# Optimization experiments

Hardware: AMD Instinct MI355X
Metric: run time of the kernel (lower is better)

Reference implementation:

```python
import jax, jax.numpy as jnp
import numpy as np

B, C = 4096, 10000
TAU = 1.0
MIN_K, MAX_K = 30, 100


def setup_inputs() -> dict:
    key = jax.random.key(0)
    k1, k2 = jax.random.split(key, 2)
    logit = jax.random.normal(k1, (B, C), dtype=jnp.float32)
    target = jax.random.randint(k2, (B,), 0, C)
    # long-tailed class counts: exponential decay from 1000 down to 5
    cls_num = np.exp(np.linspace(np.log(1000.0), np.log(5.0), C)).astype(np.float32)
    cls_num_ratio = cls_num / cls_num.sum()
    log_cls_num = jnp.asarray(np.log(cls_num_ratio + 1e-6), dtype=jnp.float32)
    freq = (cls_num.max() / cls_num).astype(np.float32)
    freq_norm = (freq - freq.min()) / (freq.max() - freq.min() + 1e-6)
    k_per_class = jnp.asarray((freq_norm * (MAX_K - MIN_K) + MIN_K).astype(np.int32))
    return {"logit": logit, "target": target, "log_cls_num": log_cls_num,
            "k_per_class": k_per_class}


def reference(logit, target, log_cls_num, k_per_class):
    b, c = logit.shape
    rows = jnp.arange(b)
    # logit-adjusted cross entropy (loss_full)
    logit_adj = logit + TAU * log_cls_num[None, :]
    log_p_adj = jax.nn.log_softmax(logit_adj, axis=1)  # [B, C]
    loss_full = -jnp.mean(log_p_adj[rows, target])
    # per-row variable-k top-k mask on the ORIGINAL logits
    prob_adj = jnp.exp(log_p_adj)
    k = jnp.minimum(k_per_class[target], c)            # [B]
    sorted_desc = -jnp.sort(-logit, axis=1)            # [B, C] descending
    thresh = sorted_desc[rows, k - 1]                  # k-th largest per row
    mask = logit >= thresh[:, None]
    masked_prob = jnp.where(mask, prob_adj, 0.0) + 1e-6
    masked_prob = masked_prob / masked_prob.sum(axis=1, keepdims=True)
    loss_topk = -jnp.mean(jnp.log(masked_prob)[rows, target])
    return 0.5 * loss_full + 0.5 * loss_topk
```

## Files before the change

kernel.cpp:

```cpp
#include <hip/hip_runtime.h>

#define BLOCK 256
#define WPB 4
#define C_DIM 10000
#define C4 (C_DIM / 4)
#define NIT4 ((C4 + 63) / 64)
#define TAU 1.0f
#define CAP 512
#define PIV_HI 2.0f
#define PIV_LO 1.0f

__device__ __forceinline__ unsigned flip_key(float f) {
    unsigned u = __float_as_uint(f);
    return (u & 0x80000000u) ? ~u : (u | 0x80000000u);
}
__device__ __forceinline__ float unflip_key(unsigned k) {
    unsigned u = (k & 0x80000000u) ? (k & 0x7fffffffu) : ~k;
    return __uint_as_float(u);
}
__device__ __forceinline__ int mbcnt64(unsigned long long m) {
    return (int)__builtin_amdgcn_mbcnt_hi((unsigned)(m >> 32),
               __builtin_amdgcn_mbcnt_lo((unsigned)(m & 0xffffffffu), 0u));
}

__global__ void zero_out_kernel(float* out, int n) {
    int i = blockIdx.x * blockDim.x + threadIdx.x;
    if (i < n) out[i] = 0.f;
}

__device__ __forceinline__ void wave_pick(uint4 hv, int lane, int shift,
                                          unsigned& prefix, unsigned& kr, unsigned& cnt) {
    unsigned loc = hv.x + hv.y + hv.z + hv.w;
    unsigned suf = loc;
    #pragma unroll
    for (int off = 1; off < 64; off <<= 1) {
        unsigned o = (unsigned)__shfl_down((int)suf, off);
        if (lane + off < 64) suf += o;
    }
    unsigned sufex = suf - loc;
    unsigned s3 = sufex + hv.w;
    unsigned s2 = s3 + hv.z;
    unsigned s1 = s2 + hv.y;
    unsigned s0 = s1 + hv.x;
    int bsel = -1; unsigned nkr = 0u, ncnt = 0u;
    if      (s3 >= kr && s3 - hv.w < kr) { bsel = 4 * lane + 3; nkr = kr - (s3 - hv.w); ncnt = hv.w; }
    else if (s2 >= kr && s2 - hv.z < kr) { bsel = 4 * lane + 2; nkr = kr - (s2 - hv.z); ncnt = hv.z; }
    else if (s1 >= kr && s1 - hv.y < kr) { bsel = 4 * lane + 1; nkr = kr - (s1 - hv.y); ncnt = hv.y; }
    else if (s0 >= kr && s0 - hv.x < kr) { bsel = 4 * lane + 0; nkr = kr - (s0 - hv.x); ncnt = hv.x; }
    unsigned long long pm = __ballot(bsel >= 0);
    int src = __ffsll((unsigned long long)pm) - 1;
    prefix |= ((unsigned)__shfl(bsel, src)) << shift;
    kr  = (unsigned)__shfl((int)nkr, src);
    cnt = (unsigned)__shfl((int)ncnt, src);
}

__global__ __launch_bounds__(BLOCK, 4) void topk_la_loss_kernel(
    const float* __restrict__ logit, const int* __restrict__ target,
    const float* __restrict__ lcn, const int* __restrict__ kpc,
    float* __restrict__ out, int B) {
    __shared__ unsigned candk[WPB][CAP];
    __shared__ unsigned short candi[WPB][CAP];
    __shared__ unsigned hist[WPB][256];

    const int tid = threadIdx.x;
    const int lane = tid & 63;
    const int wid = tid >> 6;
    const int row = blockIdx.x * WPB + wid;
    if (row >= B) return;

    const float* lrow = logit + (size_t)row * C_DIM;
    unsigned* ck = candk[wid];
    unsigned short* ci = candi[wid];
    unsigned* h = hist[wid];

    const int t = target[row];
    int k = kpc[t]; if (k > C_DIM) k = C_DIM;

    float z = 0.f, madj = -__builtin_inff();
    unsigned nb = 0u;
    #pragma unroll 2
    for (int it = 0; it < NIT4; ++it) {
        const int j4 = it * 64 + lane;
        float4 f, l;
        if (j4 < C4) {
            f = ((const float4*)lrow)[j4];
            l = ((const float4*)lcn)[j4];
        } else {
            f = make_float4(-1e30f, -1e30f, -1e30f, -1e30f);
            l = make_float4(0.f, 0.f, 0.f, 0.f);
        }
        const float a0 = f.x + TAU * l.x, a1 = f.y + TAU * l.y;
        const float a2 = f.z + TAU * l.z, a3 = f.w + TAU * l.w;
        z += __expf(a0) + __expf(a1) + __expf(a2) + __expf(a3);
        madj = fmaxf(madj, fmaxf(fmaxf(a0, a1), fmaxf(a2, a3)));
        const int j = 4 * j4;
        unsigned long long m;
        m = __ballot(f.x >= PIV_HI);
        if (f.x >= PIV_HI) { unsigned p = nb + (unsigned)mbcnt64(m); if (p < CAP) { ck[p] = __float_as_uint(f.x); ci[p] = (unsigned short)(j + 0); } }
        nb += (unsigned)__popcll(m);
        m = __ballot(f.y >= PIV_HI);
        if (f.y >= PIV_HI) { unsigned p = nb + (unsigned)mbcnt64(m); if (p < CAP) { ck[p] = __float_as_uint(f.y); ci[p] = (unsigned short)(j + 1); } }
        nb += (unsigned)__popcll(m);
        m = __ballot(f.z >= PIV_HI);
        if (f.z >= PIV_HI) { unsigned p = nb + (unsigned)mbcnt64(m); if (p < CAP) { ck[p] = __float_as_uint(f.z); ci[p] = (unsigned short)(j + 2); } }
        nb += (unsigned)__popcll(m);
        m = __ballot(f.w >= PIV_HI);
        if (f.w >= PIV_HI) { unsigned p = nb + (unsigned)mbcnt64(m); if (p < CAP) { ck[p] = __float_as_uint(f.w); ci[p] = (unsigned short)(j + 3); } }
        nb += (unsigned)__popcll(m);
    }
    #pragma unroll
    for (int off = 32; off; off >>= 1) madj = fmaxf(madj, __shfl_xor(madj, off));

    unsigned n = nb;
    int path = (n >= (unsigned)k && n <= CAP) ? 0 : ((n < (unsigned)k) ? 1 : 2);

    if (path == 1) {
        nb = 0u;
        for (int it = 0; it < NIT4; ++it) {
            const int j4 = it * 64 + lane;
            float4 f;
            if (j4 < C4) f = ((const float4*)lrow)[j4];
            else f = make_float4(-1e30f, -1e30f, -1e30f, -1e30f);
            const int j = 4 * j4;
            unsigned long long m;
            m = __ballot(f.x >= PIV_LO);
            if (f.x >= PIV_LO) { unsigned p = nb + (unsigned)mbcnt64(m); if (p < CAP) { ck[p] = __float_as_uint(f.x); ci[p] = (unsigned short)(j + 0); } }
            nb += (unsigned)__popcll(m);
            m = __ballot(f.y >= PIV_LO);
            if (f.y >= PIV_LO) { unsigned p = nb + (unsigned)mbcnt64(m); if (p < CAP) { ck[p] = __float_as_uint(f.y); ci[p] = (unsigned short)(j + 1); } }
            nb += (unsigned)__popcll(m);
            m = __ballot(f.z >= PIV_LO);
            if (f.z >= PIV_LO) { unsigned p = nb + (unsigned)mbcnt64(m); if (p < CAP) { ck[p] = __float_as_uint(f.z); ci[p] = (unsigned short)(j + 2); } }
            nb += (unsigned)__popcll(m);
            m = __ballot(f.w >= PIV_LO);
            if (f.w >= PIV_LO) { unsigned p = nb + (unsigned)mbcnt64(m); if (p < CAP) { ck[p] = __float_as_uint(f.w); ci[p] = (unsigned short)(j + 3); } }
            nb += (unsigned)__popcll(m);
        }
        n = nb;
        path = (n >= (unsigned)k && n <= CAP) ? 0 : 2;
    }

    float thresh;
    if (path == 0) {
        const int nc = (int)n;
        unsigned prefix = 0u, kr = (unsigned)k, cnt = n, kmask = 0u;
        for (int q = 0; q < 4; ++q) {
            if (cnt == 1u) break;
            const int shift = 24 - 8 * q;
            *(uint4*)&h[4 * lane] = make_uint4(0u, 0u, 0u, 0u);
            for (int i = lane; i < nc; i += 64) {
                unsigned kk = ck[i];
                if ((kk & kmask) == prefix) atomicAdd(&h[(kk >> shift) & 0xFFu], 1u);
            }
            uint4 hv = *(const uint4*)&h[4 * lane];
            wave_pick(hv, lane, shift, prefix, kr, cnt);
            kmask |= (0xFFu << shift);
        }
        if (cnt == 1u && kmask != 0xFFFFFFFFu) {
            unsigned found = 0u;
            for (int i = lane; i < nc; i += 64) {
                unsigned kk = ck[i];
                if ((kk & kmask) == prefix) found = kk;
            }
            #pragma unroll
            for (int off = 32; off; off >>= 1) found |= (unsigned)__shfl_xor((int)found, off);
            prefix = found;
        }
        thresh = __uint_as_float(prefix);
    } else {
        unsigned prefix = 0u, kr = (unsigned)k, cnt = 0u;
        for (int p = 0; p < 4; ++p) {
            const int shift = 24 - 8 * p;
            const unsigned pmask = p ? (0xFFFFFFFFu << (shift + 8)) : 0u;
            *(uint4*)&h[4 * lane] = make_uint4(0u, 0u, 0u, 0u);
            for (int it = 0; it < NIT4; ++it) {
                const int j4 = it * 64 + lane;
                if (j4 < C4) {
                    float4 f = ((const float4*)lrow)[j4];
                    unsigned kk;
                    kk = flip_key(f.x); if ((kk & pmask) == prefix) atomicAdd(&h[(kk >> shift) & 0xFFu], 1u);
                    kk = flip_key(f.y); if ((kk & pmask) == prefix) atomicAdd(&h[(kk >> shift) & 0xFFu], 1u);
                    kk = flip_key(f.z); if ((kk & pmask) == prefix) atomicAdd(&h[(kk >> shift) & 0xFFu], 1u);
                    kk = flip_key(f.w); if ((kk & pmask) == prefix) atomicAdd(&h[(kk >> shift) & 0xFFu], 1u);
                }
            }
            uint4 hv = *(const uint4*)&h[4 * lane];
            wave_pick(hv, lane, shift, prefix, kr, cnt);
        }
        thresh = unflip_key(prefix);
    }

    const bool rare = fabsf(madj) > 80.f;
    float sm = 0.f;
    if (!rare) {
        if (path == 0) {
            const int nc = (int)n;
            for (int i = lane; i < nc; i += 64) {
                const float v = __uint_as_float(ck[i]);
                if (v >= thresh) sm += __expf(v + TAU * lcn[ci[i]]);
            }
        } else {
            for (int it = 0; it < NIT4; ++it) {
                const int j4 = it * 64 + lane;
                if (j4 < C4) {
                    float4 f = ((const float4*)lrow)[j4];
                    float4 l = ((const float4*)lcn)[j4];
                    if (f.x >= thresh) sm += __expf(f.x + TAU * l.x);
                    if (f.y >= thresh) sm += __expf(f.y + TAU * l.y);
                    if (f.z >= thresh) sm += __expf(f.z + TAU * l.z);
                    if (f.w >= thresh) sm += __expf(f.w + TAU * l.w);
                }
            }
        }
    } else {
        z = 0.f;
        for (int it = 0; it < NIT4; ++it) {
            const int j4 = it * 64 + lane;
            if (j4 < C4) {
                float4 f = ((const float4*)lrow)[j4];
                float4 l = ((const float4*)lcn)[j4];
                float e;
                e = __expf(f.x + TAU * l.x - madj); z += e; if (f.x >= thresh) sm += e;
                e = __expf(f.y + TAU * l.y - madj); z += e; if (f.y >= thresh) sm += e;
                e = __expf(f.z + TAU * l.z - madj); z += e; if (f.z >= thresh) sm += e;
                e = __expf(f.w + TAU * l.w - madj); z += e; if (f.w >= thresh) sm += e;
            }
        }
    }

    #pragma unroll
    for (int off = 32; off; off >>= 1) {
        z  += __shfl_down(z, off);
        sm += __shfl_down(sm, off);
    }
    if (lane == 0) {
        const float Z = z, S = sm;
        const float logit_t = lrow[t];
        const float adj_t = logit_t + TAU * lcn[t];
        const float sub = rare ? madj : 0.f;
        const float lpt = adj_t - sub - __logf(Z);
        const float p_num = ((logit_t >= thresh) ? __expf(lpt) : 0.f) + 1e-6f;
        const float Smask = S / Z + (float)C_DIM * 1e-6f;
        const float loss = 0.5f * (-lpt + __logf(Smask) - __logf(p_num));
        atomicAdd(out, loss / (float)B);
    }
}

extern "C" void kernel_launch(void* const* d_in, const int* in_sizes, int n_in,
                              void* d_out, int out_size, void* d_ws, size_t ws_size,
                              hipStream_t stream) {
    const float* logit  = (const float*)d_in[0];
    const int*   target = (const int*)d_in[1];
    const float* lcn    = (const float*)d_in[2];
    const int*   kpc    = (const int*)d_in[3];
    float* out = (float*)d_out;
    const int B = in_sizes[1];

    zero_out_kernel<<<1, 64, 0, stream>>>(out, out_size);
    const int nblk = (B + WPB - 1) / WPB;
    topk_la_loss_kernel<<<nblk, BLOCK, 0, stream>>>(logit, target, lcn, kpc, out, B);
}
```

Before: 286.7 us.

## Split each row across four waves with block-level candidate merge

Each row now gets a full block of four waves instead of one wave. Each wave scans a quarter of the columns and collects its own threshold candidates, and shared-memory reductions then combine the max, candidate counts, Z and S. Wave 0 alone selects the threshold over the merged candidate lists. Launch bounds also change to allow more blocks per CU. This adds block syncs, and wave 0 runs the radix selection while the other three waves sit idle. The fallback full-row histogram path also runs on one wave only.

```diff
diff --git a/kernel.cpp b/kernel.cpp
--- a/kernel.cpp
+++ b/kernel.cpp
@@ -4,6 +4,8 @@
 #define WPB 4
 #define C_DIM 10000
 #define C4 (C_DIM / 4)
+#define SEGQ (C4 / WPB)
+#define ITQ ((SEGQ + 63) / 64)
 #define NIT4 ((C4 + 63) / 64)
 #define TAU 1.0f
 #define CAP 512
@@ -54,37 +56,39 @@
     cnt = (unsigned)__shfl((int)ncnt, src);
 }
 
-__global__ __launch_bounds__(BLOCK, 4) void topk_la_loss_kernel(
+__global__ __launch_bounds__(BLOCK, 8) void topk_la_loss_kernel(
     const float* __restrict__ logit, const int* __restrict__ target,
     const float* __restrict__ lcn, const int* __restrict__ kpc,
     float* __restrict__ out, int B) {
     __shared__ unsigned candk[WPB][CAP];
     __shared__ unsigned short candi[WPB][CAP];
-    __shared__ unsigned hist[WPB][256];
+    __shared__ unsigned hist[256];
+    __shared__ unsigned sh_nb[WPB];
+    __shared__ float red_a[WPB], red_b[WPB];
+    __shared__ float sh_thresh;
 
     const int tid = threadIdx.x;
     const int lane = tid & 63;
     const int wid = tid >> 6;
-    const int row = blockIdx.x * WPB + wid;
-    if (row >= B) return;
-
+    const int row = blockIdx.x;
     const float* lrow = logit + (size_t)row * C_DIM;
+
+    const int t = target[row];
+    int k = kpc[t]; if (k > C_DIM) k = C_DIM;
+
     unsigned* ck = candk[wid];
     unsigned short* ci = candi[wid];
-    unsigned* h = hist[wid];
-
-    const int t = target[row];
-    int k = kpc[t]; if (k > C_DIM) k = C_DIM;
+    const int base4 = wid * SEGQ;
 
     float z = 0.f, madj = -__builtin_inff();
     unsigned nb = 0u;
     #pragma unroll 2
-    for (int it = 0; it < NIT4; ++it) {
-        const int j4 = it * 64 + lane;
+    for (int it = 0; it < ITQ; ++it) {
+        const int j4l = it * 64 + lane;
         float4 f, l;
-        if (j4 < C4) {
-            f = ((const float4*)lrow)[j4];
-            l = ((const float4*)lcn)[j4];
+        if (j4l < SEGQ) {
+            f = ((const float4*)lrow)[base4 + j4l];
+            l = ((const float4*)lcn)[base4 + j4l];
         } else {
             f = make_float4(-1e30f, -1e30f, -1e30f, -1e30f);
             l = make_float4(0.f, 0.f, 0.f, 0.f);
@@ -93,7 +97,7 @@
         const float a2 = f.z + TAU * l.z, a3 = f.w + TAU * l.w;
         z += __expf(a0) + __expf(a1) + __expf(a2) + __expf(a3);
         madj = fmaxf(madj, fmaxf(fmaxf(a0, a1), fmaxf(a2, a3)));
-        const int j = 4 * j4;
+        const int j = 4 * (base4 + j4l);
         unsigned long long m;
         m = __ballot(f.x >= PIV_HI);
         if (f.x >= PIV_HI) { unsigned p = nb + (unsigned)mbcnt64(m); if (p < CAP) { ck[p] = __float_as_uint(f.x); ci[p] = (unsigned short)(j + 0); } }
@@ -110,18 +114,23 @@
     }
     #pragma unroll
     for (int off = 32; off; off >>= 1) madj = fmaxf(madj, __shfl_xor(madj, off));
-
-    unsigned n = nb;
-    int path = (n >= (unsigned)k && n <= CAP) ? 0 : ((n < (unsigned)k) ? 1 : 2);
+    if (lane == 0) { red_a[wid] = madj; sh_nb[wid] = nb; }
+    __syncthreads();
+
+    const float madjB = fmaxf(fmaxf(red_a[0], red_a[1]), fmaxf(red_a[2], red_a[3]));
+    unsigned nbs0 = sh_nb[0], nbs1 = sh_nb[1], nbs2 = sh_nb[2], nbs3 = sh_nb[3];
+    unsigned ntot = nbs0 + nbs1 + nbs2 + nbs3;
+    unsigned nmax = max(max(nbs0, nbs1), max(nbs2, nbs3));
+    int path = (ntot >= (unsigned)k && nmax <= CAP) ? 0 : ((ntot < (unsigned)k) ? 1 : 2);
 
     if (path == 1) {
         nb = 0u;
-        for (int it = 0; it < NIT4; ++it) {
-            const int j4 = it * 64 + lane;
+        for (int it = 0; it < ITQ; ++it) {
+            const int j4l = it * 64 + lane;
             float4 f;
-            if (j4 < C4) f = ((const float4*)lrow)[j4];
+            if (j4l < SEGQ) f = ((const float4*)lrow)[base4 + j4l];
             else f = make_float4(-1e30f, -1e30f, -1e30f, -1e30f);
-            const int j = 4 * j4;
+            const int j = 4 * (base4 + j4l);
             unsigned long long m;
             m = __ballot(f.x >= PIV_LO);
             if (f.x >= PIV_LO) { unsigned p = nb + (unsigned)mbcnt64(m); if (p < CAP) { ck[p] = __float_as_uint(f.x); ci[p] = (unsigned short)(j + 0); } }
@@ -136,75 +145,90 @@
             if (f.w >= PIV_LO) { unsigned p = nb + (unsigned)mbcnt64(m); if (p < CAP) { ck[p] = __float_as_uint(f.w); ci[p] = (unsigned short)(j + 3); } }
             nb += (unsigned)__popcll(m);
         }
-        n = nb;
-        path = (n >= (unsigned)k && n <= CAP) ? 0 : 2;
-    }
-
-    float thresh;
+        if (lane == 0) sh_nb[wid] = nb;
+        __syncthreads();
+        nbs0 = sh_nb[0]; nbs1 = sh_nb[1]; nbs2 = sh_nb[2]; nbs3 = sh_nb[3];
+        ntot = nbs0 + nbs1 + nbs2 + nbs3;
+        nmax = max(max(nbs0, nbs1), max(nbs2, nbs3));
+        path = (ntot >= (unsigned)k && nmax <= CAP) ? 0 : 2;
+    }
+
     if (path == 0) {
-        const int nc = (int)n;
-        unsigned prefix = 0u, kr = (unsigned)k, cnt = n, kmask = 0u;
-        for (int q = 0; q < 4; ++q) {
-            if (cnt == 1u) break;
-            const int shift = 24 - 8 * q;
-            *(uint4*)&h[4 * lane] = make_uint4(0u, 0u, 0u, 0u);
-            for (int i = lane; i < nc; i += 64) {
-                unsigned kk = ck[i];
-                if ((kk & kmask) == prefix) atomicAdd(&h[(kk >> shift) & 0xFFu], 1u);
-            }
-            uint4 hv = *(const uint4*)&h[4 * lane];
-            wave_pick(hv, lane, shift, prefix, kr, cnt);
-            kmask |= (0xFFu << shift);
-        }
-        if (cnt == 1u && kmask != 0xFFFFFFFFu) {
-            unsigned found = 0u;
-            for (int i = lane; i < nc; i += 64) {
-                unsigned kk = ck[i];
-                if ((kk & kmask) == prefix) found = kk;
-            }
-            #pragma unroll
-            for (int off = 32; off; off >>= 1) found |= (unsigned)__shfl_xor((int)found, off);
-            prefix = found;
-        }
-        thresh = __uint_as_float(prefix);
+        if (wid == 0) {
+            unsigned prefix = 0u, kr = (unsigned)k, cnt = ntot, kmask = 0u;
+            const unsigned nbs[4] = {nbs0, nbs1, nbs2, nbs3};
+            for (int q = 0; q < 4; ++q) {
+                if (cnt == 1u) break;
+                const int shift = 24 - 8 * q;
+                *(uint4*)&hist[4 * lane] = make_uint4(0u, 0u, 0u, 0u);
+                #pragma unroll
+                for (int s = 0; s < 4; ++s) {
+                    for (int i = lane; i < (int)nbs[s]; i += 64) {
+                        unsigned kk = candk[s][i];
+                        if ((kk & kmask) == prefix) atomicAdd(&hist[(kk >> shift) & 0xFFu], 1u);
+                    }
+                }
+                uint4 hv = *(const uint4*)&hist[4 * lane];
+                wave_pick(hv, lane, shift, prefix, kr, cnt);
+                kmask |= (0xFFu << shift);
+            }
+            if (cnt == 1u && kmask != 0xFFFFFFFFu) {
+                unsigned found = 0u;
+                #pragma unroll
+                for (int s = 0; s < 4; ++s) {
+                    for (int i = lane; i < (int)nbs[s]; i += 64) {
+                        unsigned kk = candk[s][i];
+                        if ((kk & kmask) == prefix) found = kk;
+                    }
+                }
+                #pragma unroll
+                for (int off = 32; off; off >>= 1) found |= (unsigned)__shfl_xor((int)found, off);
+                prefix = found;
+            }
+            if (lane == 0) sh_thresh = __uint_as_float(prefix);
+        }
     } else {
-        unsigned prefix = 0u, kr = (unsigned)k, cnt = 0u;
-        for (int p = 0; p < 4; ++p) {
-            const int shift = 24 - 8 * p;
-            const unsigned pmask = p ? (0xFFFFFFFFu << (shift + 8)) : 0u;
-            *(uint4*)&h[4 * lane] = make_uint4(0u, 0u, 0u, 0u);
-            for (int it = 0; it < NIT4; ++it) {
-                const int j4 = it * 64 + lane;
-                if (j4 < C4) {
-                    float4 f = ((const float4*)lrow)[j4];
-                    unsigned kk;
-                    kk = flip_key(f.x); if ((kk & pmask) == prefix) atomicAdd(&h[(kk >> shift) & 0xFFu], 1u);
-                    kk = flip_key(f.y); if ((kk & pmask) == prefix) atomicAdd(&h[(kk >> shift) & 0xFFu], 1u);
-                    kk = flip_key(f.z); if ((kk & pmask) == prefix) atomicAdd(&h[(kk >> shift) & 0xFFu], 1u);
-                    kk = flip_key(f.w); if ((kk & pmask) == prefix) atomicAdd(&h[(kk >> shift) & 0xFFu], 1u);
-                }
-            }
-            uint4 hv = *(const uint4*)&h[4 * lane];
-            wave_pick(hv, lane, shift, prefix, kr, cnt);
-        }
-        thresh = unflip_key(prefix);
-    }
-
-    const bool rare = fabsf(madj) > 80.f;
+        if (wid == 0) {
+            unsigned prefix = 0u, kr = (unsigned)k, cnt = 0u;
+            for (int p = 0; p < 4; ++p) {
+                const int shift = 24 - 8 * p;
+                const unsigned pmask = p ? (0xFFFFFFFFu << (shift + 8)) : 0u;
+                *(uint4*)&hist[4 * lane] = make_uint4(0u, 0u, 0u, 0u);
+                for (int it = 0; it < NIT4; ++it) {
+                    const int j4 = it * 64 + lane;
+                    if (j4 < C4) {
+                        float4 f = ((const float4*)lrow)[j4];
+                        unsigned kk;
+                        kk = flip_key(f.x); if ((kk & pmask) == prefix) atomicAdd(&hist[(kk >> shift) & 0xFFu], 1u);
+                        kk = flip_key(f.y); if ((kk & pmask) == prefix) atomicAdd(&hist[(kk >> shift) & 0xFFu], 1u);
+                        kk = flip_key(f.z); if ((kk & pmask) == prefix) atomicAdd(&hist[(kk >> shift) & 0xFFu], 1u);
+                        kk = flip_key(f.w); if ((kk & pmask) == prefix) atomicAdd(&hist[(kk >> shift) & 0xFFu], 1u);
+                    }
+                }
+                uint4 hv = *(const uint4*)&hist[4 * lane];
+                wave_pick(hv, lane, shift, prefix, kr, cnt);
+            }
+            if (lane == 0) sh_thresh = unflip_key(prefix);
+        }
+    }
+    __syncthreads();
+    const float thresh = sh_thresh;
+
+    const bool rare = fabsf(madjB) > 80.f;
     float sm = 0.f;
     if (!rare) {
         if (path == 0) {
-            const int nc = (int)n;
+            const int nc = (int)sh_nb[wid];
             for (int i = lane; i < nc; i += 64) {
                 const float v = __uint_as_float(ck[i]);
                 if (v >= thresh) sm += __expf(v + TAU * lcn[ci[i]]);
             }
         } else {
-            for (int it = 0; it < NIT4; ++it) {
-                const int j4 = it * 64 + lane;
-                if (j4 < C4) {
-                    float4 f = ((const float4*)lrow)[j4];
-                    float4 l = ((const float4*)lcn)[j4];
+            for (int it = 0; it < ITQ; ++it) {
+                const int j4l = it * 64 + lane;
+                if (j4l < SEGQ) {
+                    float4 f = ((const float4*)lrow)[base4 + j4l];
+                    float4 l = ((const float4*)lcn)[base4 + j4l];
                     if (f.x >= thresh) sm += __expf(f.x + TAU * l.x);
                     if (f.y >= thresh) sm += __expf(f.y + TAU * l.y);
                     if (f.z >= thresh) sm += __expf(f.z + TAU * l.z);
@@ -214,16 +238,16 @@
         }
     } else {
         z = 0.f;
-        for (int it = 0; it < NIT4; ++it) {
-            const int j4 = it * 64 + lane;
-            if (j4 < C4) {
-                float4 f = ((const float4*)lrow)[j4];
-                float4 l = ((const float4*)lcn)[j4];
+        for (int it = 0; it < ITQ; ++it) {
+            const int j4l = it * 64 + lane;
+            if (j4l < SEGQ) {
+                float4 f = ((const float4*)lrow)[base4 + j4l];
+                float4 l = ((const float4*)lcn)[base4 + j4l];
                 float e;
-                e = __expf(f.x + TAU * l.x - madj); z += e; if (f.x >= thresh) sm += e;
-                e = __expf(f.y + TAU * l.y - madj); z += e; if (f.y >= thresh) sm += e;
-                e = __expf(f.z + TAU * l.z - madj); z += e; if (f.z >= thresh) sm += e;
-                e = __expf(f.w + TAU * l.w - madj); z += e; if (f.w >= thresh) sm += e;
+                e = __expf(f.x + TAU * l.x - madjB); z += e; if (f.x >= thresh) sm += e;
+                e = __expf(f.y + TAU * l.y - madjB); z += e; if (f.y >= thresh) sm += e;
+                e = __expf(f.z + TAU * l.z - madjB); z += e; if (f.z >= thresh) sm += e;
+                e = __expf(f.w + TAU * l.w - madjB); z += e; if (f.w >= thresh) sm += e;
             }
         }
     }
@@ -233,11 +257,15 @@
         z  += __shfl_down(z, off);
         sm += __shfl_down(sm, off);
     }
-    if (lane == 0) {
-        const float Z = z, S = sm;
+    if (lane == 0) { red_a[wid] = z; red_b[wid] = sm; }
+    __syncthreads();
+
+    if (tid == 0) {
+        const float Z = red_a[0] + red_a[1] + red_a[2] + red_a[3];
+        const float S = red_b[0] + red_b[1] + red_b[2] + red_b[3];
         const float logit_t = lrow[t];
         const float adj_t = logit_t + TAU * lcn[t];
-        const float sub = rare ? madj : 0.f;
+        const float sub = rare ? madjB : 0.f;
         const float lpt = adj_t - sub - __logf(Z);
         const float p_num = ((logit_t >= thresh) ? __expf(lpt) : 0.f) + 1e-6f;
         const float Smask = S / Z + (float)C_DIM * 1e-6f;
@@ -257,6 +285,5 @@
     const int B = in_sizes[1];
 
     zero_out_kernel<<<1, 64, 0, stream>>>(out, out_size);
-    const int nblk = (B + WPB - 1) / WPB;
-    topk_la_loss_kernel<<<nblk, BLOCK, 0, stream>>>(logit, target, lcn, kpc, out, B);
-}
+    topk_la_loss_kernel<<<B, BLOCK, 0, stream>>>(logit, target, lcn, kpc, out, B);
+}
```

Result: faster. 262.0 us (-8.6%).
